# Optimization experiments

Hardware: AMD Instinct MI355X
Metric: run time of the kernel (lower is better)

The kernel has to match this reference:

```python
import jax, jax.numpy as jnp
from jax import lax
import numpy as np

B, T, F, H, O = 512, 256, 256, 512, 1


def setup_inputs() -> dict:
    key = jax.random.key(0)
    ks = jax.random.split(key, 8)
    s = 1.0 / np.sqrt(H)  # PyTorch LSTMCell init scale
    x = jax.random.normal(ks[0], (B, T, F), dtype=jnp.float32)
    W_ih = jax.random.uniform(ks[1], (4 * H, F), minval=-s, maxval=s, dtype=jnp.float32)
    W_hh = jax.random.uniform(ks[2], (4 * H, H), minval=-s, maxval=s, dtype=jnp.float32)
    b_ih = jax.random.uniform(ks[3], (4 * H,), minval=-s, maxval=s, dtype=jnp.float32)
    b_hh = jax.random.uniform(ks[4], (4 * H,), minval=-s, maxval=s, dtype=jnp.float32)
    so = 1.0 / np.sqrt(H)
    W_out = jax.random.uniform(ks[5], (O, H), minval=-so, maxval=so, dtype=jnp.float32)
    b_out = jax.random.uniform(ks[6], (O,), minval=-so, maxval=so, dtype=jnp.float32)
    return {"x": x, "W_ih": W_ih, "W_hh": W_hh, "b_ih": b_ih, "b_hh": b_hh,
            "W_out": W_out, "b_out": b_out}


def reference(x, W_ih, W_hh, b_ih, b_hh, W_out, b_out):
    # x: [B, T, F]; single shared LSTMCell scanned over T steps (zero init state),
    # then linear head on the LAST hidden state (torch.cat in the original is a no-op).
    Bq = x.shape[0]
    Hq = W_hh.shape[1]

    def step(carry, xt):
        h, c = carry
        gates = xt @ W_ih.T + b_ih + h @ W_hh.T + b_hh  # [B, 4H]
        i, f, g, o = jnp.split(gates, 4, axis=-1)       # PyTorch gate order: i, f, g, o
        i = jax.nn.sigmoid(i)
        f = jax.nn.sigmoid(f)
        g = jnp.tanh(g)
        o = jax.nn.sigmoid(o)
        c = f * c + i * g
        h = o * jnp.tanh(c)
        return (h, c), None

    h0 = jnp.zeros((Bq, Hq), dtype=x.dtype)
    (h, _), _ = lax.scan(step, (h0, h0), jnp.swapaxes(x, 0, 1))  # scan over time [T,B,F]
    return h @ W_out.T + b_out  # [B, O]
```

## Files before the change

kernel.cpp:

```cpp
#include <hip/hip_runtime.h>
#include <stdint.h>

typedef unsigned int u32;
typedef unsigned short u16;
typedef __attribute__((ext_vector_type(8))) __bf16 bf16x8;
typedef __attribute__((ext_vector_type(4))) float f32x4;
typedef __attribute__((ext_vector_type(4))) u32 u32x4;
typedef __attribute__((ext_vector_type(2))) u32 u32x2;

#define NSTEPS 256
#define XB_BYTES   67108864u
#define SL_OFF     XB_BYTES
#define GRP_BYTES   65536u
#define SLOT_BYTES  524288u
#define CNT_OFF    (SL_OFF + 2u * SLOT_BYTES)
#define LDS_TOTAL 98304

static __device__ __forceinline__ u16 f2bf(float f) {
  u32 u = __builtin_bit_cast(u32, f);
  return (u16)((u + 0x7fffu + ((u >> 16) & 1u)) >> 16);
}
static __device__ __forceinline__ float bf2f(u16 h) {
  u32 u = ((u32)h) << 16;
  return __builtin_bit_cast(float, u);
}
static __device__ __forceinline__ float sigm(float x) {
  return __builtin_amdgcn_rcpf(1.f + __builtin_amdgcn_exp2f(-1.4426950408889634f * x));
}
static __device__ __forceinline__ float tanh_(float x) {
  return 1.f - 2.f * __builtin_amdgcn_rcpf(1.f + __builtin_amdgcn_exp2f(2.8853900817779268f * x));
}

static __device__ __forceinline__ u32 poll_sc(const u32* p) {
  u32 v;
  asm volatile("global_load_dword %0, %1, off sc0 sc1\n\t"
               "s_waitcnt vmcnt(0)"
               : "=v"(v) : "v"(p) : "memory");
  return v;
}
static __device__ __forceinline__ void st8_sc(void* p, u32x2 v) {
  asm volatile("global_store_dwordx2 %0, %1, off sc0 sc1" :: "v"(p), "v"(v) : "memory");
}
static __device__ __forceinline__ u32x4 ld16_sc_wait(const void* p) {
  u32x4 v;
  asm volatile("global_load_dwordx4 %0, %1, off sc0 sc1\n\t"
               "s_waitcnt vmcnt(0)"
               : "=v"(v) : "v"(p) : "memory");
  return v;
}
static __device__ __forceinline__ void xissue(u32x4 x[8], const void* base) {
  asm volatile(
    "global_load_dwordx4 %0, %8, off offset:0\n\t"
    "global_load_dwordx4 %1, %8, off offset:64\n\t"
    "global_load_dwordx4 %2, %8, off offset:128\n\t"
    "global_load_dwordx4 %3, %8, off offset:192\n\t"
    "global_load_dwordx4 %4, %8, off offset:256\n\t"
    "global_load_dwordx4 %5, %8, off offset:320\n\t"
    "global_load_dwordx4 %6, %8, off offset:384\n\t"
    "global_load_dwordx4 %7, %8, off offset:448"
    : "=&v"(x[0]), "=&v"(x[1]), "=&v"(x[2]), "=&v"(x[3]),
      "=&v"(x[4]), "=&v"(x[5]), "=&v"(x[6]), "=&v"(x[7])
    : "v"(base) : "memory");
}
static __device__ __forceinline__ void aissue(u32x4 s[16], const char* b) {
  asm volatile(
    "global_load_dwordx4 %0, %16, off sc0 sc1\n\t"
    "global_load_dwordx4 %1, %17, off sc0 sc1\n\t"
    "global_load_dwordx4 %2, %18, off sc0 sc1\n\t"
    "global_load_dwordx4 %3, %19, off sc0 sc1\n\t"
    "global_load_dwordx4 %4, %20, off sc0 sc1\n\t"
    "global_load_dwordx4 %5, %21, off sc0 sc1\n\t"
    "global_load_dwordx4 %6, %22, off sc0 sc1\n\t"
    "global_load_dwordx4 %7, %23, off sc0 sc1\n\t"
    "global_load_dwordx4 %8, %24, off sc0 sc1\n\t"
    "global_load_dwordx4 %9, %25, off sc0 sc1\n\t"
    "global_load_dwordx4 %10, %26, off sc0 sc1\n\t"
    "global_load_dwordx4 %11, %27, off sc0 sc1\n\t"
    "global_load_dwordx4 %12, %28, off sc0 sc1\n\t"
    "global_load_dwordx4 %13, %29, off sc0 sc1\n\t"
    "global_load_dwordx4 %14, %30, off sc0 sc1\n\t"
    "global_load_dwordx4 %15, %31, off sc0 sc1"
    : "=&v"(s[0]), "=&v"(s[1]), "=&v"(s[2]), "=&v"(s[3]),
      "=&v"(s[4]), "=&v"(s[5]), "=&v"(s[6]), "=&v"(s[7]),
      "=&v"(s[8]), "=&v"(s[9]), "=&v"(s[10]), "=&v"(s[11]),
      "=&v"(s[12]), "=&v"(s[13]), "=&v"(s[14]), "=&v"(s[15])
    : "v"(b), "v"(b + 4096), "v"(b + 8192), "v"(b + 12288),
      "v"(b + 16384), "v"(b + 20480), "v"(b + 24576), "v"(b + 28672),
      "v"(b + 32768), "v"(b + 36864), "v"(b + 40960), "v"(b + 45056),
      "v"(b + 49152), "v"(b + 53248), "v"(b + 57344), "v"(b + 61440)
    : "memory");
}
#define AWAIT(N) do { asm volatile("s_waitcnt vmcnt(" #N ")" ::: "memory"); \
                      __builtin_amdgcn_sched_barrier(0); } while (0)

__global__ void cvt_x(const float* __restrict__ x, u16* __restrict__ xb) {
  int i = blockIdx.x * 256 + threadIdx.x;
  float4 v = ((const float4*)x)[i];
  ushort4 o;
  o.x = f2bf(v.x); o.y = f2bf(v.y); o.z = f2bf(v.z); o.w = f2bf(v.w);
  ((ushort4*)xb)[i] = o;
}

__global__ void __launch_bounds__(256, 1) lstm_main(
    const u16* __restrict__ xb,
    const float* __restrict__ W_ih, const float* __restrict__ W_hh,
    const float* __restrict__ b_ih, const float* __restrict__ b_hh,
    const float* __restrict__ W_out, const float* __restrict__ b_out,
    float* __restrict__ out, char* __restrict__ ws)
{
  __shared__ char smem[LDS_TOTAL];
  const int tid = threadIdx.x;
  const int wg  = blockIdx.x;
  const int grp = wg & 7;
  const int wgN = wg >> 3;
  const int lane = tid & 63;
  const int wv   = tid >> 6;
  const int cc = lane & 15;
  const int hi = lane >> 4;

  {
    const int lane_in = tid & 63;
    const int lc = lane_in & 15, hh = lane_in >> 4;
    #pragma unroll
    for (int nt = 0; nt < 4; ++nt)
      #pragma unroll
      for (int it = 0; it < 6; ++it) {
        int kcc = (tid >> 6) + it * 4;
        int n = nt * 512 + wgN * 16 + lc;
        int k = kcc * 32 + hh * 8;
        float4 v0, v1;
        if (kcc < 8) {
          v0 = *(const float4*)(W_ih + n * 256 + k);
          v1 = *(const float4*)(W_ih + n * 256 + k + 4);
        } else {
          int k2 = k - 256;
          v0 = *(const float4*)(W_hh + n * 512 + k2);
          v1 = *(const float4*)(W_hh + n * 512 + k2 + 4);
        }
        u32x4 g;
        g[0] = (u32)f2bf(v0.x) | ((u32)f2bf(v0.y) << 16);
        g[1] = (u32)f2bf(v0.z) | ((u32)f2bf(v0.w) << 16);
        g[2] = (u32)f2bf(v1.x) | ((u32)f2bf(v1.y) << 16);
        g[3] = (u32)f2bf(v1.z) | ((u32)f2bf(v1.w) << 16);
        *(u32x4*)(smem + ((nt * 24 + kcc) * 64 + lane_in) * 16) = g;
      }
  }

  float bvn[4][4];
  #pragma unroll
  for (int nt = 0; nt < 4; ++nt)
    #pragma unroll
    for (int r = 0; r < 4; ++r) {
      int n = nt * 512 + wgN * 16 + hi * 4 + r;
      bvn[nt][r] = b_ih[n] + b_hh[n];
    }

  u32* cnt = (u32*)(ws + CNT_OFF + grp * 128);
  char* slices = ws + SL_OFF;
  const char* grpsl = slices + (size_t)grp * GRP_BYTES;

  const u16* xrow = xb + (size_t)(grp * 64 + wv * 16 + cc) * 65536 + hi * 8;
  const int afrag = (hi >> 1) * 2048 + (wv * 16 + cc) * 32 + (hi & 1) * 16;

  __syncthreads();

  bf16x8 bh[16][4];
  #pragma unroll
  for (int kc = 0; kc < 16; ++kc)
    #pragma unroll
    for (int nt = 0; nt < 4; ++nt)
      bh[kc][nt] = *(const bf16x8*)(smem + ((nt * 24 + kc + 8) * 64 + lane) * 16);
  #pragma unroll
  for (int kc = 0; kc < 16; ++kc)
    #pragma unroll
    for (int nt = 0; nt < 4; ++nt)
      asm volatile("" : "+v"(bh[kc][nt]));

  float cst[4] = {0.f, 0.f, 0.f, 0.f};

  u32x4 xreg[8];
  xissue(xreg, xrow);

  #pragma unroll 1
  for (int t = 0; t < NSTEPS; ++t) {
    if (t > 0) {
      u32 tgt = 32u * (u32)t;
      while (poll_sc(cnt) < tgt) __builtin_amdgcn_s_sleep(1);
    }

    const char* rds = grpsl + (size_t)((t & 1) ^ 1) * SLOT_BYTES;
    u32x4 av[16];
    aissue(av, rds + afrag);

    AWAIT(16);
    f32x4 acc[4] = {};
    #pragma unroll
    for (int kc = 0; kc < 8; ++kc) {
      bf16x8 b = __builtin_bit_cast(bf16x8, xreg[kc]);
      #pragma unroll
      for (int nt = 0; nt < 4; ++nt) {
        bf16x8 a = *(const bf16x8*)(smem + ((nt * 24 + kc) * 64 + lane) * 16);
        acc[nt] = __builtin_amdgcn_mfma_f32_16x16x32_bf16(a, b, acc[nt], 0, 0, 0);
      }
    }

    AWAIT(12);
    #pragma unroll
    for (int kc = 0; kc < 4; ++kc) {
      bf16x8 b = __builtin_bit_cast(bf16x8, av[kc]);
      #pragma unroll
      for (int nt = 0; nt < 4; ++nt)
        acc[nt] = __builtin_amdgcn_mfma_f32_16x16x32_bf16(bh[kc][nt], b, acc[nt], 0, 0, 0);
    }
    AWAIT(8);
    #pragma unroll
    for (int kc = 4; kc < 8; ++kc) {
      bf16x8 b = __builtin_bit_cast(bf16x8, av[kc]);
      #pragma unroll
      for (int nt = 0; nt < 4; ++nt)
        acc[nt] = __builtin_amdgcn_mfma_f32_16x16x32_bf16(bh[kc][nt], b, acc[nt], 0, 0, 0);
    }
    AWAIT(4);
    #pragma unroll
    for (int kc = 8; kc < 12; ++kc) {
      bf16x8 b = __builtin_bit_cast(bf16x8, av[kc]);
      #pragma unroll
      for (int nt = 0; nt < 4; ++nt)
        acc[nt] = __builtin_amdgcn_mfma_f32_16x16x32_bf16(bh[kc][nt], b, acc[nt], 0, 0, 0);
    }
    AWAIT(0);
    #pragma unroll
    for (int kc = 12; kc < 16; ++kc) {
      bf16x8 b = __builtin_bit_cast(bf16x8, av[kc]);
      #pragma unroll
      for (int nt = 0; nt < 4; ++nt)
        acc[nt] = __builtin_amdgcn_mfma_f32_16x16x32_bf16(bh[kc][nt], b, acc[nt], 0, 0, 0);
    }

    char* wdst = slices + (size_t)(t & 1) * SLOT_BYTES + grp * GRP_BYTES + wgN * 2048;
    u32 plo = 0, phi2 = 0;
    #pragma unroll
    for (int r = 0; r < 4; ++r) {
      float gi = acc[0][r] + bvn[0][r];
      float gf = acc[1][r] + bvn[1][r];
      float gg = acc[2][r] + bvn[2][r];
      float go = acc[3][r] + bvn[3][r];
      float ii = sigm(gi), ff = sigm(gf), g2 = tanh_(gg), oo = sigm(go);
      float cn = ff * cst[r] + ii * g2;
      cst[r] = cn;
      float hn = oo * tanh_(cn);
      u32 hb = (u32)f2bf(hn);
      if (r < 2) plo |= hb << (16 * r);
      else       phi2 |= hb << (16 * (r - 2));
    }
    u32x2 pk; pk[0] = plo; pk[1] = phi2;
    st8_sc(wdst + (wv * 16 + cc) * 32 + hi * 8, pk);

    AWAIT(0);
    __syncthreads();
    if (tid == 0) atomicAdd(cnt, 1u);
    if (t + 1 < NSTEPS)
      xissue(xreg, xrow + (size_t)(t + 1) * 256);
  }

  if (wgN == 0) {
    while (poll_sc(cnt) < 32u * NSTEPS) __builtin_amdgcn_s_sleep(1);
    const char* src = grpsl + SLOT_BYTES;
    int b = tid >> 2, q = tid & 3;
    float s = 0.f;
    #pragma unroll
    for (int j16 = 0; j16 < 8; ++j16) {
      int nblk = q * 8 + j16;
      const char* p = src + nblk * 2048 + b * 32;
      u32x4 w0 = ld16_sc_wait(p);
      u32x4 w1 = ld16_sc_wait(p + 16);
      #pragma unroll
      for (int d = 0; d < 4; ++d) {
        int jb = q * 128 + j16 * 16 + d * 2;
        s += bf2f((u16)(w0[d] & 0xffff)) * W_out[jb];
        s += bf2f((u16)(w0[d] >> 16))    * W_out[jb + 1];
        s += bf2f((u16)(w1[d] & 0xffff)) * W_out[jb + 8];
        s += bf2f((u16)(w1[d] >> 16))    * W_out[jb + 9];
      }
    }
    s += __shfl_xor(s, 1);
    s += __shfl_xor(s, 2);
    if (q == 0) out[grp * 64 + b] = s + b_out[0];
  }
}

extern "C" void kernel_launch(void* const* d_in, const int* in_sizes, int n_in,
                              void* d_out, int out_size, void* d_ws, size_t ws_size,
                              hipStream_t stream) {
  (void)in_sizes; (void)n_in; (void)out_size; (void)ws_size;
  const float* x     = (const float*)d_in[0];
  const float* W_ih  = (const float*)d_in[1];
  const float* W_hh  = (const float*)d_in[2];
  const float* b_ih  = (const float*)d_in[3];
  const float* b_hh  = (const float*)d_in[4];
  const float* W_out = (const float*)d_in[5];
  const float* b_out = (const float*)d_in[6];
  char* ws = (char*)d_ws;

  hipMemsetAsync(ws + SL_OFF, 0, 2u * SLOT_BYTES + 1024u, stream);
  cvt_x<<<32768, 256, 0, stream>>>(x, (u16*)ws);
  lstm_main<<<256, 256, 0, stream>>>((const u16*)ws, W_ih, W_hh, b_ih, b_hh,
                                     W_out, b_out, (float*)d_out, ws);
}
```

Before: 1.122 ms.

## Replace per-group counter barrier with per-wave tag flags and peeled first step

Swaps the workgroup __syncthreads plus single atomic counter per group for per-wave tag arrays: each wave increments its own tag after storing h, and each wave polls the 32 producer tags it depends on using a wave-wide __all. The first timestep is peeled so it skips the h@W_hh part entirely (h0 is zero), which also allows a much smaller memset covering only the tag area. This removes the block-wide barrier and counter contention on the recurrent critical path. In exchange each wave issues more polling traffic, and a guard that breaks out after a bounded spin could let a wave proceed on stale data.

```diff
diff --git a/kernel.cpp b/kernel.cpp
--- a/kernel.cpp
+++ b/kernel.cpp
@@ -13,7 +13,7 @@
 #define SL_OFF     XB_BYTES
 #define GRP_BYTES   65536u
 #define SLOT_BYTES  524288u
-#define CNT_OFF    (SL_OFF + 2u * SLOT_BYTES)
+#define TAG_OFF    (SL_OFF + 2u * SLOT_BYTES)
 #define LDS_TOTAL 98304
 
 static __device__ __forceinline__ u16 f2bf(float f) {
@@ -33,8 +33,7 @@
 
 static __device__ __forceinline__ u32 poll_sc(const u32* p) {
   u32 v;
-  asm volatile("global_load_dword %0, %1, off sc0 sc1\n\t"
-               "s_waitcnt vmcnt(0)"
+  asm volatile("global_load_dword %0, %1, off sc0 sc1\n\ts_waitcnt vmcnt(0)"
                : "=v"(v) : "v"(p) : "memory");
   return v;
 }
@@ -43,8 +42,7 @@
 }
 static __device__ __forceinline__ u32x4 ld16_sc_wait(const void* p) {
   u32x4 v;
-  asm volatile("global_load_dwordx4 %0, %1, off sc0 sc1\n\t"
-               "s_waitcnt vmcnt(0)"
+  asm volatile("global_load_dwordx4 %0, %1, off sc0 sc1\n\ts_waitcnt vmcnt(0)"
                : "=v"(v) : "v"(p) : "memory");
   return v;
 }
@@ -93,6 +91,15 @@
 #define AWAIT(N) do { asm volatile("s_waitcnt vmcnt(" #N ")" ::: "memory"); \
                       __builtin_amdgcn_sched_barrier(0); } while (0)
 
+static __device__ __forceinline__ void wait_tags(const u32* p, u32 want) {
+  int guard = 0;
+  u32 v = poll_sc(p);
+  while (!__all((int)(v >= want))) {
+    if (++guard > (1 << 16)) break;
+    v = poll_sc(p);
+  }
+}
+
 __global__ void cvt_x(const float* __restrict__ x, u16* __restrict__ xb) {
   int i = blockIdx.x * 256 + threadIdx.x;
   float4 v = ((const float4*)x)[i];
@@ -119,13 +126,12 @@
   const int hi = lane >> 4;
 
   {
-    const int lane_in = tid & 63;
-    const int lc = lane_in & 15, hh = lane_in >> 4;
+    const int lc = lane & 15, hh = lane >> 4;
     #pragma unroll
     for (int nt = 0; nt < 4; ++nt)
       #pragma unroll
       for (int it = 0; it < 6; ++it) {
-        int kcc = (tid >> 6) + it * 4;
+        int kcc = wv + it * 4;
         int n = nt * 512 + wgN * 16 + lc;
         int k = kcc * 32 + hh * 8;
         float4 v0, v1;
@@ -142,7 +148,7 @@
         g[1] = (u32)f2bf(v0.z) | ((u32)f2bf(v0.w) << 16);
         g[2] = (u32)f2bf(v1.x) | ((u32)f2bf(v1.y) << 16);
         g[3] = (u32)f2bf(v1.z) | ((u32)f2bf(v1.w) << 16);
-        *(u32x4*)(smem + ((nt * 24 + kcc) * 64 + lane_in) * 16) = g;
+        *(u32x4*)(smem + ((nt * 24 + kcc) * 64 + lane) * 16) = g;
       }
   }
 
@@ -155,12 +161,16 @@
       bvn[nt][r] = b_ih[n] + b_hh[n];
     }
 
-  u32* cnt = (u32*)(ws + CNT_OFF + grp * 128);
   char* slices = ws + SL_OFF;
   const char* grpsl = slices + (size_t)grp * GRP_BYTES;
-
+  const size_t myoff = (size_t)grp * GRP_BYTES + wgN * 2048 + (wv * 16 + cc) * 32 + hi * 8;
+  const size_t rdoff = (size_t)grp * GRP_BYTES
+                     + (hi >> 1) * 2048 + (wv * 16 + cc) * 32 + (hi & 1) * 16;
   const u16* xrow = xb + (size_t)(grp * 64 + wv * 16 + cc) * 65536 + hi * 8;
-  const int afrag = (hi >> 1) * 2048 + (wv * 16 + cc) * 32 + (hi & 1) * 16;
+
+  u32* tagplane = (u32*)(ws + TAG_OFF + grp * 512 + wv * 128);
+  const u32* mypoll = tagplane + (lane & 31);
+  u32* mytag = tagplane + wgN;
 
   __syncthreads();
 
@@ -180,19 +190,8 @@
 
   u32x4 xreg[8];
   xissue(xreg, xrow);
-
-  #pragma unroll 1
-  for (int t = 0; t < NSTEPS; ++t) {
-    if (t > 0) {
-      u32 tgt = 32u * (u32)t;
-      while (poll_sc(cnt) < tgt) __builtin_amdgcn_s_sleep(1);
-    }
-
-    const char* rds = grpsl + (size_t)((t & 1) ^ 1) * SLOT_BYTES;
-    u32x4 av[16];
-    aissue(av, rds + afrag);
-
-    AWAIT(16);
+  AWAIT(0);
+  {
     f32x4 acc[4] = {};
     #pragma unroll
     for (int kc = 0; kc < 8; ++kc) {
@@ -203,41 +202,6 @@
         acc[nt] = __builtin_amdgcn_mfma_f32_16x16x32_bf16(a, b, acc[nt], 0, 0, 0);
       }
     }
-
-    AWAIT(12);
-    #pragma unroll
-    for (int kc = 0; kc < 4; ++kc) {
-      bf16x8 b = __builtin_bit_cast(bf16x8, av[kc]);
-      #pragma unroll
-      for (int nt = 0; nt < 4; ++nt)
-        acc[nt] = __builtin_amdgcn_mfma_f32_16x16x32_bf16(bh[kc][nt], b, acc[nt], 0, 0, 0);
-    }
-    AWAIT(8);
-    #pragma unroll
-    for (int kc = 4; kc < 8; ++kc) {
-      bf16x8 b = __builtin_bit_cast(bf16x8, av[kc]);
-      #pragma unroll
-      for (int nt = 0; nt < 4; ++nt)
-        acc[nt] = __builtin_amdgcn_mfma_f32_16x16x32_bf16(bh[kc][nt], b, acc[nt], 0, 0, 0);
-    }
-    AWAIT(4);
-    #pragma unroll
-    for (int kc = 8; kc < 12; ++kc) {
-      bf16x8 b = __builtin_bit_cast(bf16x8, av[kc]);
-      #pragma unroll
-      for (int nt = 0; nt < 4; ++nt)
-        acc[nt] = __builtin_amdgcn_mfma_f32_16x16x32_bf16(bh[kc][nt], b, acc[nt], 0, 0, 0);
-    }
-    AWAIT(0);
-    #pragma unroll
-    for (int kc = 12; kc < 16; ++kc) {
-      bf16x8 b = __builtin_bit_cast(bf16x8, av[kc]);
-      #pragma unroll
-      for (int nt = 0; nt < 4; ++nt)
-        acc[nt] = __builtin_amdgcn_mfma_f32_16x16x32_bf16(bh[kc][nt], b, acc[nt], 0, 0, 0);
-    }
-
-    char* wdst = slices + (size_t)(t & 1) * SLOT_BYTES + grp * GRP_BYTES + wgN * 2048;
     u32 plo = 0, phi2 = 0;
     #pragma unroll
     for (int r = 0; r < 4; ++r) {
@@ -254,21 +218,102 @@
       else       phi2 |= hb << (16 * (r - 2));
     }
     u32x2 pk; pk[0] = plo; pk[1] = phi2;
-    st8_sc(wdst + (wv * 16 + cc) * 32 + hi * 8, pk);
-
+    st8_sc(slices + myoff, pk);
     AWAIT(0);
-    __syncthreads();
-    if (tid == 0) atomicAdd(cnt, 1u);
+    if (lane == 0) atomicAdd(mytag, 1u);
+    xissue(xreg, xrow + 256);
+  }
+
+  #pragma unroll 1
+  for (int t = 1; t < NSTEPS; ++t) {
+    wait_tags(mypoll, (u32)t);
+
+    const char* rds = slices + (size_t)((t - 1) & 1) * SLOT_BYTES + rdoff;
+    u32x4 av[16];
+    aissue(av, rds);
+
+    f32x4 acc[4] = {};
+    #pragma unroll
+    for (int kc = 0; kc < 8; ++kc) {
+      bf16x8 b = __builtin_bit_cast(bf16x8, xreg[kc]);
+      #pragma unroll
+      for (int nt = 0; nt < 4; ++nt) {
+        bf16x8 a = *(const bf16x8*)(smem + ((nt * 24 + kc) * 64 + lane) * 16);
+        acc[nt] = __builtin_amdgcn_mfma_f32_16x16x32_bf16(a, b, acc[nt], 0, 0, 0);
+      }
+    }
+
+    AWAIT(12);
+    #pragma unroll
+    for (int kc = 0; kc < 4; ++kc) {
+      bf16x8 b = __builtin_bit_cast(bf16x8, av[kc]);
+      #pragma unroll
+      for (int nt = 0; nt < 4; ++nt)
+        acc[nt] = __builtin_amdgcn_mfma_f32_16x16x32_bf16(bh[kc][nt], b, acc[nt], 0, 0, 0);
+    }
+    AWAIT(8);
+    #pragma unroll
+    for (int kc = 4; kc < 8; ++kc) {
+      bf16x8 b = __builtin_bit_cast(bf16x8, av[kc]);
+      #pragma unroll
+      for (int nt = 0; nt < 4; ++nt)
+        acc[nt] = __builtin_amdgcn_mfma_f32_16x16x32_bf16(bh[kc][nt], b, acc[nt], 0, 0, 0);
+    }
+    AWAIT(4);
+    #pragma unroll
+    for (int kc = 8; kc < 12; ++kc) {
+      bf16x8 b = __builtin_bit_cast(bf16x8, av[kc]);
+      #pragma unroll
+      for (int nt = 0; nt < 4; ++nt)
+        acc[nt] = __builtin_amdgcn_mfma_f32_16x16x32_bf16(bh[kc][nt], b, acc[nt], 0, 0, 0);
+    }
+    AWAIT(0);
+    #pragma unroll
+    for (int kc = 12; kc < 16; ++kc) {
+      bf16x8 b = __builtin_bit_cast(bf16x8, av[kc]);
+      #pragma unroll
+      for (int nt = 0; nt < 4; ++nt)
+        acc[nt] = __builtin_amdgcn_mfma_f32_16x16x32_bf16(bh[kc][nt], b, acc[nt], 0, 0, 0);
+    }
+
+    u32 plo = 0, phi2 = 0;
+    #pragma unroll
+    for (int r = 0; r < 4; ++r) {
+      float gi = acc[0][r] + bvn[0][r];
+      float gf = acc[1][r] + bvn[1][r];
+      float gg = acc[2][r] + bvn[2][r];
+      float go = acc[3][r] + bvn[3][r];
+      float ii = sigm(gi), ff = sigm(gf), g2 = tanh_(gg), oo = sigm(go);
+      float cn = ff * cst[r] + ii * g2;
+      cst[r] = cn;
+      float hn = oo * tanh_(cn);
+      u32 hb = (u32)f2bf(hn);
+      if (r < 2) plo |= hb << (16 * r);
+      else       phi2 |= hb << (16 * (r - 2));
+    }
+    u32x2 pk; pk[0] = plo; pk[1] = phi2;
+    st8_sc(slices + (size_t)(t & 1) * SLOT_BYTES + myoff, pk);
+    AWAIT(0);
+    if (lane == 0) atomicAdd(mytag, 1u);
     if (t + 1 < NSTEPS)
       xissue(xreg, xrow + (size_t)(t + 1) * 256);
   }
 
   if (wgN == 0) {
-    while (poll_sc(cnt) < 32u * NSTEPS) __builtin_amdgcn_s_sleep(1);
+    {
+      const u32* tp = (const u32*)(ws + TAG_OFF + grp * 512) + (lane * 2);
+      int guard = 0;
+      for (;;) {
+        u32 v0 = poll_sc(tp);
+        u32 v1 = poll_sc(tp + 1);
+        if (__all((int)((v0 >= NSTEPS) & (v1 >= NSTEPS)))) break;
+        if (++guard > (1 << 16)) break;
+      }
+    }
     const char* src = grpsl + SLOT_BYTES;
     int b = tid >> 2, q = tid & 3;
     float s = 0.f;
-    #pragma unroll
+    #pragma unroll 1
     for (int j16 = 0; j16 < 8; ++j16) {
       int nblk = q * 8 + j16;
       const char* p = src + nblk * 2048 + b * 32;
@@ -302,7 +347,7 @@
   const float* b_out = (const float*)d_in[6];
   char* ws = (char*)d_ws;
 
-  hipMemsetAsync(ws + SL_OFF, 0, 2u * SLOT_BYTES + 1024u, stream);
+  hipMemsetAsync(ws + TAG_OFF, 0, 4096, stream);
   cvt_x<<<32768, 256, 0, stream>>>(x, (u16*)ws);
   lstm_main<<<256, 256, 0, stream>>>((const u16*)ws, W_ih, W_hh, b_ih, b_hh,
                                      W_out, b_out, (float*)d_out, ws);
```

Result: slower. 2.324 ms (+107.0%).
